# Performance work log

Hardware: AMD Instinct MI355X
Metric: run time of the kernel (lower is better)

Reference implementation:

```python
import jax, jax.numpy as jnp
import numpy as np

N_NODES = 200000
N_EDGES = 3200000
N_GRAPHS = 2000
N_MAX = 256   # max nodes per graph for dense batching (mean ~100)
K = 30        # SortAggregation k


def setup_inputs() -> dict:
    key = jax.random.key(0)
    ks = jax.random.split(key, 12)
    x = jax.random.normal(ks[0], (N_NODES, 128), jnp.float32)
    edge_index = jax.random.randint(ks[1], (2, N_EDGES), 0, N_NODES, dtype=jnp.int32)
    batch = jnp.sort(jax.random.randint(ks[2], (N_NODES,), 0, N_GRAPHS, dtype=jnp.int32))
    def lin(k, i, o):
        return (jax.random.normal(k, (i, o), jnp.float32) / np.sqrt(i)).astype(jnp.float32)
    return {
        'x': x, 'edge_index': edge_index, 'batch': batch,
        'W1': lin(ks[3], 128, 32), 'b1': jnp.zeros(32, jnp.float32),
        'W2': lin(ks[4], 32, 32),  'b2': jnp.zeros(32, jnp.float32),
        'W3': lin(ks[5], 32, 32),  'b3': jnp.zeros(32, jnp.float32),
        'W4': lin(ks[6], 32, 1),   'b4': jnp.zeros(1, jnp.float32),
        'cw5': (jax.random.normal(ks[7], (16, 1, 97), jnp.float32) / np.sqrt(97)).astype(jnp.float32),
        'cb5': jnp.zeros(16, jnp.float32),
        'cw6': (jax.random.normal(ks[8], (32, 16, 5), jnp.float32) / np.sqrt(80)).astype(jnp.float32),
        'cb6': jnp.zeros(32, jnp.float32),
        'fw1': lin(ks[9], 352, 128), 'fb1': jnp.zeros(128, jnp.float32),
        'fw2': lin(ks[10], 128, 10), 'fb2': jnp.zeros(10, jnp.float32),
    }


def _gcn_conv(h, W, b, src, dst, emask):
    # PyG GCNConv: remove self-loops handled via emask (weight 0), then add
    # self-loops weight 1; symmetric normalization D^{-1/2}(A+I)D^{-1/2} X W + b
    deg = jax.ops.segment_sum(emask, dst, num_segments=N_NODES) + 1.0  # + self loop
    dis = jax.lax.rsqrt(deg)  # deg >= 1 always, no inf
    norm = dis[src] * dis[dst] * emask  # [E]
    hw = h @ W                          # [N, out]
    agg = jax.ops.segment_sum(hw[src] * norm[:, None], dst, num_segments=N_NODES)
    agg = agg + hw * (dis * dis)[:, None]  # self-loop message
    return agg + b


def _sort_pool(x, batch):
    # PyG SortAggregation(k): dense-batch with fill = min-1, sort each graph by
    # last feature channel (descending), keep top-k rows, zero out padding, flatten.
    N, D = x.shape
    ones = jnp.ones((N,), jnp.int32)
    counts = jax.ops.segment_sum(ones, batch, num_segments=N_GRAPHS)
    offsets = jnp.concatenate([jnp.zeros((1,), jnp.int32), jnp.cumsum(counts)[:-1]])
    pos = jnp.arange(N, dtype=jnp.int32) - offsets[batch]  # batch is sorted
    fill = x.min() - 1.0
    dense = jnp.full((N_GRAPHS, N_MAX, D), fill, x.dtype).at[batch, pos].set(x)
    perm = jnp.argsort(-dense[:, :, -1], axis=1)            # descending by last channel
    dense = jnp.take_along_axis(dense, perm[:, :, None], axis=1)[:, :K]  # [G, K, D]
    dense = jnp.where(dense == fill, 0.0, dense)
    return dense.reshape(N_GRAPHS, K * D)


def _conv1d(x, w, b, stride):
    y = jax.lax.conv_general_dilated(x, w, window_strides=(stride,), padding='VALID',
                                     dimension_numbers=('NCH', 'OIH', 'NCH'))
    return y + b[None, :, None]


def reference(x, edge_index, batch, W1, b1, W2, b2, W3, b3, W4, b4,
              cw5, cb5, cw6, cb6, fw1, fb1, fw2, fb2):
    src, dst = edge_index[0], edge_index[1]
    emask = (src != dst).astype(x.dtype)  # remove_self_loops

    x1 = jnp.tanh(_gcn_conv(x,  W1, b1, src, dst, emask))
    x2 = jnp.tanh(_gcn_conv(x1, W2, b2, src, dst, emask))
    x3 = jnp.tanh(_gcn_conv(x2, W3, b3, src, dst, emask))
    x4 = jnp.tanh(_gcn_conv(x3, W4, b4, src, dst, emask))
    h = jnp.concatenate([x1, x2, x3, x4], axis=-1)  # [N, 97]

    p = _sort_pool(h, batch)                 # [G, 30*97]
    p = p[:, None, :]                        # [G, 1, 2910]
    p = jax.nn.relu(_conv1d(p, cw5, cb5, 97))  # [G, 16, 30]
    G = p.shape[0]
    p = p.reshape(G, 16, 15, 2).max(axis=-1)   # MaxPool1d(2,2) -> [G, 16, 15]
    p = jax.nn.relu(_conv1d(p, cw6, cb6, 1))   # [G, 32, 11]
    p = p.reshape(G, -1)                       # [G, 352]
    out = jax.nn.relu(p @ fw1 + fb1)           # dropout is identity at inference
    return jax.nn.log_softmax(out @ fw2 + fb2, axis=-1)
```

## Files before the change

### kernel.cpp

```cpp
#include <hip/hip_runtime.h>

#define N_NODESC 200000
#define N_EDGESC 3200000
#define N_GRAPHSC 2000
#define NMAXG 256
#define TOPK 30
#define DCAT 97
#define POOLW (TOPK*DCAT)
#define BUCKW 512
#define NBUCK ((N_NODESC+BUCKW-1)/BUCKW)
#define CAP 10240
#define PCHUNK 4096
#define NPBLK ((N_EDGESC+PCHUNK-1)/PCHUNK)

typedef int  iv4 __attribute__((ext_vector_type(4)));
typedef float fv4 __attribute__((ext_vector_type(4)));

__global__ __launch_bounds__(256) void k_part(const int* __restrict__ src, const int* __restrict__ dst,
                                              const int* __restrict__ batch, int* __restrict__ gcount,
                                              int* __restrict__ bcur, unsigned* __restrict__ pairbuf){
  __shared__ int hcnt[NBUCK];
  __shared__ int hbase[NBUCK];
  __shared__ int lofs[NBUCK];
  __shared__ int scan[256];
  __shared__ unsigned lbuf[PCHUNK];
  __shared__ unsigned short bbuf[PCHUNK];
  int blk = blockIdx.x, t = threadIdx.x;
  int nd = blk*256 + t;
  if (nd < N_NODESC) atomicAdd(&gcount[batch[nd]],1);
  int e0 = blk*PCHUNK;
  int e1 = e0 + PCHUNK; if (e1 > N_EDGESC) e1 = N_EDGESC;
  for (int i=t;i<NBUCK;i+=256) hcnt[i]=0;
  unsigned pk[16]; unsigned meta[16];
  __syncthreads();
  #pragma unroll
  for (int i=0;i<4;i++){
    int e = e0 + i*1024 + t*4;
    if (e < e1){
      iv4 d4 = __builtin_nontemporal_load((const iv4*)(dst+e));
      iv4 s4 = __builtin_nontemporal_load((const iv4*)(src+e));
      #pragma unroll
      for (int k=0;k<4;k++){
        int d = (k==0)?d4.x:(k==1)?d4.y:(k==2)?d4.z:d4.w;
        int s = (k==0)?s4.x:(k==1)?s4.y:(k==2)?s4.z:s4.w;
        if (s!=d){
          int bk = d>>9;
          int pl = atomicAdd(&hcnt[bk],1);
          pk[i*4+k]   = ((unsigned)(d&511)<<18)|(unsigned)s;
          meta[i*4+k] = ((unsigned)bk<<13)|(unsigned)pl;
        } else meta[i*4+k] = 0xFFFFFFFFu;
      }
    } else {
      #pragma unroll
      for (int k=0;k<4;k++) meta[i*4+k] = 0xFFFFFFFFu;
    }
  }
  __syncthreads();
  int i0=2*t, i1=2*t+1;
  int h0 = (i0<NBUCK)? hcnt[i0] : 0;
  int h1 = (i1<NBUCK)? hcnt[i1] : 0;
  int sp = h0+h1;
  scan[t]=sp; __syncthreads();
  for (int off=1;off<256;off<<=1){
    int u = (t>=off)? scan[t-off] : 0;
    __syncthreads();
    scan[t]+=u;
    __syncthreads();
  }
  int ex = scan[t]-sp;
  if (i0<NBUCK) lofs[i0]=ex;
  if (i1<NBUCK) lofs[i1]=ex+h0;
  for (int i=t;i<NBUCK;i+=256){
    int c = hcnt[i];
    hbase[i] = c ? (i*CAP + atomicAdd(&bcur[i],c)) : 0;
  }
  __syncthreads();
  #pragma unroll
  for (int k=0;k<16;k++){
    unsigned m = meta[k];
    if (m != 0xFFFFFFFFu){
      int bk = (int)(m>>13);
      int j = lofs[bk] + (int)(m & 0x1FFFu);
      lbuf[j] = pk[k];
      bbuf[j] = (unsigned short)bk;
    }
  }
  __syncthreads();
  int tot = lofs[NBUCK-1] + hcnt[NBUCK-1];
  for (int j=t; j<tot; j+=256){
    int bk = bbuf[j];
    int addr = hbase[bk] + (j - lofs[bk]);
    if (addr < (bk+1)*CAP) pairbuf[addr] = lbuf[j];
  }
}

__global__ __launch_bounds__(512) void k_bsort(const unsigned* __restrict__ pairbuf, const int* __restrict__ bcur,
                                               int* __restrict__ degc, int* __restrict__ offs,
                                               float* __restrict__ dis, int* __restrict__ csr){
  __shared__ int lcsr[CAP];
  __shared__ int lcnt[512];
  __shared__ int lofs[512];
  __shared__ int lcur[512];
  __shared__ int red[512];
  int b = blockIdx.x, t = threadIdx.x;
  int cnt_b = bcur[b]; if (cnt_b > CAP) cnt_b = CAP;
  int pv = 0;
  if (t < b){ int c = bcur[t]; if (c>CAP) c=CAP; pv = c; }
  red[t]=pv; __syncthreads();
  for (int off=256;off>0;off>>=1){ if (t<off) red[t]+=red[t+off]; __syncthreads(); }
  int base = red[0];
  const unsigned* pb = pairbuf + (size_t)b*CAP;
  lcnt[t]=0; __syncthreads();
  for (int i=t;i<cnt_b;i+=512) atomicAdd(&lcnt[pb[i]>>18],1);
  __syncthreads();
  lofs[t]=lcnt[t]; __syncthreads();
  for (int off=1;off<512;off<<=1){
    int u = (t>=off)? lofs[t-off] : 0;
    __syncthreads();
    lofs[t]+=u;
    __syncthreads();
  }
  int excl = lofs[t]-lcnt[t];
  int node = b*BUCKW + t;
  if (node < N_NODESC){
    degc[node] = lcnt[t];
    offs[node] = base + excl;
    dis[node]  = rsqrtf((float)lcnt[t] + 1.0f);
  }
  lcur[t]=excl;
  __syncthreads();
  for (int i=t;i<cnt_b;i+=512){
    unsigned v = pb[i];
    int p = atomicAdd(&lcur[v>>18],1);
    lcsr[p] = (int)(v & 0x3FFFFu);
  }
  __syncthreads();
  for (int i=t;i<cnt_b;i+=512) csr[base+i]=lcsr[i];
}

template<int KIN>
__global__ __launch_bounds__(256) void k_mm(const float* __restrict__ X, const float* __restrict__ W,
                                            const float* __restrict__ dis, float* __restrict__ out){
  __shared__ float xs[256*33];
  int r0 = blockIdx.x*256;
  int t = threadIdx.x;
  int r = r0 + t;
  float acc[32];
  #pragma unroll
  for (int f=0;f<32;f++) acc[f]=0.f;
  for (int kc=0; kc<KIN; kc+=32){
    __syncthreads();
    #pragma unroll
    for (int it=0; it<8; it++){
      int idx = it*256 + t;
      int row = idx>>3, c4 = idx&7;
      int gr = r0 + row;
      fv4 v = {0.f,0.f,0.f,0.f};
      if (gr < N_NODESC) v = __builtin_nontemporal_load((const fv4*)(X + (size_t)gr*KIN + kc + c4*4));
      int bofs = row*33 + c4*4;
      xs[bofs]=v.x; xs[bofs+1]=v.y; xs[bofs+2]=v.z; xs[bofs+3]=v.w;
    }
    __syncthreads();
    const float* w0 = W + kc*32;
    const float* xrow = xs + t*33;
    #pragma unroll
    for (int k=0;k<32;k++){
      float xv = xrow[k];
      #pragma unroll
      for (int f=0;f<32;f++) acc[f] = fmaf(xv, w0[k*32+f], acc[f]);
    }
  }
  if (r >= N_NODESC) return;
  float d = dis[r];
  float4* op = (float4*)(out + (size_t)r*32);
  #pragma unroll
  for (int f4=0;f4<8;f4++)
    op[f4] = make_float4(acc[4*f4]*d, acc[4*f4+1]*d, acc[4*f4+2]*d, acc[4*f4+3]*d);
}

__global__ __launch_bounds__(256) void k_agg(const float* __restrict__ hws, const int* __restrict__ csr,
                      const int* __restrict__ off, const int* __restrict__ cnt,
                      const float* __restrict__ dis, const float* __restrict__ bias,
                      float* __restrict__ out){
  int t = blockIdx.x*256 + threadIdx.x;
  int n = t>>5;
  if (n>=N_NODESC) return;
  int f = t&31;
  int beg = off[n], c = cnt[n];
  float a0=0.f,a1=0.f,a2=0.f,a3=0.f,a4=0.f,a5=0.f,a6=0.f,a7=0.f;
  for (int base=0; base<c; base+=32){
    int m = c-base; if (m>32) m=32;
    int idx = (f<m)? csr[beg+base+f] : 0;
    int j=0;
    for (; j+8<=m; j+=8){
      int s0=__shfl(idx,j,32),   s1=__shfl(idx,j+1,32),
          s2=__shfl(idx,j+2,32), s3=__shfl(idx,j+3,32),
          s4=__shfl(idx,j+4,32), s5=__shfl(idx,j+5,32),
          s6=__shfl(idx,j+6,32), s7=__shfl(idx,j+7,32);
      float v0=hws[(size_t)s0*32+f];
      float v1=hws[(size_t)s1*32+f];
      float v2=hws[(size_t)s2*32+f];
      float v3=hws[(size_t)s3*32+f];
      float v4=hws[(size_t)s4*32+f];
      float v5=hws[(size_t)s5*32+f];
      float v6=hws[(size_t)s6*32+f];
      float v7=hws[(size_t)s7*32+f];
      a0+=v0; a1+=v1; a2+=v2; a3+=v3; a4+=v4; a5+=v5; a6+=v6; a7+=v7;
    }
    for (; j+4<=m; j+=4){
      int s0=__shfl(idx,j,32), s1=__shfl(idx,j+1,32),
          s2=__shfl(idx,j+2,32), s3=__shfl(idx,j+3,32);
      float v0=hws[(size_t)s0*32+f];
      float v1=hws[(size_t)s1*32+f];
      float v2=hws[(size_t)s2*32+f];
      float v3=hws[(size_t)s3*32+f];
      a0+=v0; a1+=v1; a2+=v2; a3+=v3;
    }
    for (; j<m; j++){
      int s0=__shfl(idx,j,32);
      a0 += hws[(size_t)s0*32+f];
    }
  }
  float dn = dis[n];
  float sum = ((a0+a1)+(a2+a3)) + ((a4+a5)+(a6+a7));
  float v = dn*(sum+hws[(size_t)n*32+f]) + bias[f];
  out[(size_t)n*32+f] = tanhf(v);
}

__global__ __launch_bounds__(256) void k_aggF1(const float* __restrict__ hws, const int* __restrict__ csr,
                      const int* __restrict__ off, const int* __restrict__ cnt,
                      const float* __restrict__ dis, const float* __restrict__ bias,
                      const float* __restrict__ W4,
                      float* __restrict__ xout, float* __restrict__ hw4){
  __shared__ float Ws[32];
  int t = threadIdx.x;
  if (t<32) Ws[t]=W4[t];
  __syncthreads();
  int gt = blockIdx.x*256 + t;
  int n = gt>>5;
  if (n>=N_NODESC) return;
  int f = gt&31;
  int beg = off[n], c = cnt[n];
  float a0=0.f,a1=0.f,a2=0.f,a3=0.f,a4=0.f,a5=0.f,a6=0.f,a7=0.f;
  for (int base=0; base<c; base+=32){
    int m = c-base; if (m>32) m=32;
    int idx = (f<m)? csr[beg+base+f] : 0;
    int j=0;
    for (; j+8<=m; j+=8){
      int s0=__shfl(idx,j,32),   s1=__shfl(idx,j+1,32),
          s2=__shfl(idx,j+2,32), s3=__shfl(idx,j+3,32),
          s4=__shfl(idx,j+4,32), s5=__shfl(idx,j+5,32),
          s6=__shfl(idx,j+6,32), s7=__shfl(idx,j+7,32);
      float v0=hws[(size_t)s0*32+f];
      float v1=hws[(size_t)s1*32+f];
      float v2=hws[(size_t)s2*32+f];
      float v3=hws[(size_t)s3*32+f];
      float v4=hws[(size_t)s4*32+f];
      float v5=hws[(size_t)s5*32+f];
      float v6=hws[(size_t)s6*32+f];
      float v7=hws[(size_t)s7*32+f];
      a0+=v0; a1+=v1; a2+=v2; a3+=v3; a4+=v4; a5+=v5; a6+=v6; a7+=v7;
    }
    for (; j+4<=m; j+=4){
      int s0=__shfl(idx,j,32), s1=__shfl(idx,j+1,32),
          s2=__shfl(idx,j+2,32), s3=__shfl(idx,j+3,32);
      float v0=hws[(size_t)s0*32+f];
      float v1=hws[(size_t)s1*32+f];
      float v2=hws[(size_t)s2*32+f];
      float v3=hws[(size_t)s3*32+f];
      a0+=v0; a1+=v1; a2+=v2; a3+=v3;
    }
    for (; j<m; j++){
      int s0=__shfl(idx,j,32);
      a0 += hws[(size_t)s0*32+f];
    }
  }
  float dn = dis[n];
  float sum = ((a0+a1)+(a2+a3)) + ((a4+a5)+(a6+a7));
  float xv = tanhf(dn*(sum+hws[(size_t)n*32+f]) + bias[f]);
  xout[(size_t)n*32+f] = xv;
  float acc = xv*Ws[f];
  #pragma unroll
  for (int off2=16;off2>0;off2>>=1) acc += __shfl_xor(acc, off2, 32);
  if (f==0) hw4[n] = acc*dn;
}

__global__ void k_agg4(const float* __restrict__ hws4, const int* __restrict__ csr,
                       const int* __restrict__ off, const int* __restrict__ cnt,
                       const float* __restrict__ dis, const float* __restrict__ b4,
                       float* __restrict__ x4){
  int n = blockIdx.x*256+threadIdx.x;
  if (n>=N_NODESC) return;
  int beg=off[n], c=cnt[n];
  float a0=0.f,a1=0.f,a2=0.f,a3=0.f,a4=0.f,a5=0.f,a6=0.f,a7=0.f;
  int e=0;
  for (; e+8<=c; e+=8){
    int s0=csr[beg+e],   s1=csr[beg+e+1], s2=csr[beg+e+2], s3=csr[beg+e+3];
    int s4=csr[beg+e+4], s5=csr[beg+e+5], s6=csr[beg+e+6], s7=csr[beg+e+7];
    a0+=hws4[s0]; a1+=hws4[s1]; a2+=hws4[s2]; a3+=hws4[s3];
    a4+=hws4[s4]; a5+=hws4[s5]; a6+=hws4[s6]; a7+=hws4[s7];
  }
  for (; e<c; e++) a0+=hws4[csr[beg+e]];
  float dn=dis[n];
  float sum = ((a0+a1)+(a2+a3)) + ((a4+a5)+(a6+a7));
  x4[n] = tanhf(dn*(sum+hws4[n]) + b4[0]);
}

__global__ __launch_bounds__(256) void k_sortpool(const float* __restrict__ x1,const float* __restrict__ x2,const float* __restrict__ x3,const float* __restrict__ x4,
                           const int* __restrict__ gcount, float* __restrict__ pool){
  __shared__ float vals[NMAXG];
  __shared__ int sel[TOPK];
  __shared__ int redsum[256];
  int g = blockIdx.x;
  int t = threadIdx.x;
  int part = 0;
  for (int i=t; i<g; i+=256) part += gcount[i];
  redsum[t]=part; __syncthreads();
  for (int off=128;off>0;off>>=1){ if (t<off) redsum[t]+=redsum[t+off]; __syncthreads(); }
  int start = redsum[0];
  int cntg = gcount[g]; if (cntg>NMAXG) cntg=NMAXG;
  float v = 0.f;
  if (t<cntg) v = x4[start+t];
  vals[t] = v;
  __syncthreads();
  if (t<cntg){
    int rank=0;
    for (int j=0;j<cntg;j++){
      float vj=vals[j];
      rank += (vj>v) || (vj==v && j<t);
    }
    if (rank<TOPK) sel[rank]=t;
  }
  __syncthreads();
  int nsel = cntg<TOPK?cntg:TOPK;
  float* pg = pool + (size_t)g*POOLW;
  for (int idx=t; idx<POOLW; idx+=256){
    int r = idx/DCAT, c = idx - r*DCAT;
    float val=0.f;
    if (r<nsel){
      int node = start + sel[r];
      if (c<32) val = x1[(size_t)node*32+c];
      else if (c<64) val = x2[(size_t)node*32+(c-32)];
      else if (c<96) val = x3[(size_t)node*32+(c-64)];
      else val = x4[node];
    }
    pg[idx]=val;
  }
}

__global__ __launch_bounds__(128) void k_head(const float* __restrict__ pool,
                       const float* __restrict__ cw5, const float* __restrict__ cb5,
                       const float* __restrict__ cw6, const float* __restrict__ cb6,
                       const float* __restrict__ fw1, const float* __restrict__ fb1,
                       const float* __restrict__ fw2, const float* __restrict__ fb2,
                       float* __restrict__ out){
  __shared__ float P[POOLW];
  __shared__ float o5[16*30];
  __shared__ float m[16*15];
  __shared__ float o6[32*11];
  __shared__ float o1[128];
  __shared__ float logits[10];
  int g=blockIdx.x, t=threadIdx.x;
  const float* pg = pool + (size_t)g*POOLW;
  for (int i=t;i<POOLW;i+=128) P[i]=pg[i];
  __syncthreads();
  for (int i=t;i<480;i+=128){
    int o=i/30, k=i-o*30;
    float acc=cb5[o];
    const float* w=cw5+o*97;
    const float* p=P+k*97;
    for(int c=0;c<97;c++) acc = fmaf(p[c], w[c], acc);
    o5[o*30+k]=fmaxf(acc,0.f);
  }
  __syncthreads();
  for (int i=t;i<240;i+=128){
    int o=i/15,k=i-o*15;
    m[i]=fmaxf(o5[o*30+2*k], o5[o*30+2*k+1]);
  }
  __syncthreads();
  for (int i=t;i<352;i+=128){
    int o2=i/11, k=i-o2*11;
    float acc=cb6[o2];
    const float* w=cw6+o2*80;
    #pragma unroll
    for(int ii=0;ii<16;ii++)
      #pragma unroll
      for(int r=0;r<5;r++)
        acc = fmaf(m[ii*15+k+r], w[ii*5+r], acc);
    o6[o2*11+k]=fmaxf(acc,0.f);
  }
  __syncthreads();
  {
    float acc=fb1[t];
    for(int i=0;i<352;i++) acc = fmaf(o6[i], fw1[i*128+t], acc);
    o1[t]=fmaxf(acc,0.f);
  }
  __syncthreads();
  if (t<10){
    float acc=fb2[t];
    for(int j=0;j<128;j++) acc = fmaf(o1[j], fw2[j*10+t], acc);
    logits[t]=acc;
  }
  __syncthreads();
  if (t==0){
    float mx=logits[0];
    for(int c=1;c<10;c++) mx=fmaxf(mx,logits[c]);
    float s=0.f;
    for(int c=0;c<10;c++) s+=expf(logits[c]-mx);
    float lse=logf(s)+mx;
    for(int c=0;c<10;c++) out[(size_t)g*10+c]=logits[c]-lse;
  }
}

extern "C" void kernel_launch(void* const* d_in, const int* in_sizes, int n_in,
                              void* d_out, int out_size, void* d_ws, size_t ws_size,
                              hipStream_t stream){
  const float* x    = (const float*)d_in[0];
  const int*   ei   = (const int*)d_in[1];
  const int*   batch= (const int*)d_in[2];
  const float* W1=(const float*)d_in[3]; const float* b1=(const float*)d_in[4];
  const float* W2=(const float*)d_in[5]; const float* b2=(const float*)d_in[6];
  const float* W3=(const float*)d_in[7]; const float* b3=(const float*)d_in[8];
  const float* W4=(const float*)d_in[9]; const float* b4=(const float*)d_in[10];
  const float* cw5=(const float*)d_in[11]; const float* cb5=(const float*)d_in[12];
  const float* cw6=(const float*)d_in[13]; const float* cb6=(const float*)d_in[14];
  const float* fw1=(const float*)d_in[15]; const float* fb1=(const float*)d_in[16];
  const float* fw2=(const float*)d_in[17]; const float* fb2=(const float*)d_in[18];
  float* out=(float*)d_out;
  const int* src = ei;
  const int* dst = ei + N_EDGESC;

  char* ws=(char*)d_ws;
  size_t o=0;
  auto alloc=[&](size_t nbytes)->char*{ char* p=ws+o; o += (nbytes+255)&~(size_t)255; return p; };
  float* dis    = (float*)alloc((size_t)N_NODESC*4);
  int*   offs   = (int*)alloc((size_t)N_NODESC*4);
  int*   degc   = (int*)alloc((size_t)N_NODESC*4);
  int*   bcur   = (int*)alloc((size_t)NBUCK*4);
  int*   gcount = (int*)alloc((size_t)N_GRAPHSC*4);
  unsigned* pairbuf = (unsigned*)alloc((size_t)NBUCK*CAP*4);
  int*   csr    = (int*)alloc((size_t)N_EDGESC*4);
  float* x1 = (float*)alloc((size_t)N_NODESC*32*4);
  float* x2 = (float*)alloc((size_t)N_NODESC*32*4);
  float* x3 = (float*)alloc((size_t)N_NODESC*32*4);
  float* x4 = (float*)alloc((size_t)N_NODESC*4);
  float* hw = (float*)alloc((size_t)N_NODESC*32*4);
  float* hw4 = (float*)alloc((size_t)N_NODESC*4);
  float* pool = hw;

  size_t mset = (((size_t)NBUCK*4+255)&~(size_t)255) + (size_t)N_GRAPHSC*4;
  (void)hipMemsetAsync(bcur, 0, mset, stream);

  int gN = (N_NODESC+255)/256;

  k_part<<<NPBLK,256,0,stream>>>(src,dst,batch,gcount,bcur,pairbuf);
  k_bsort<<<NBUCK,512,0,stream>>>(pairbuf,bcur,degc,offs,dis,csr);

  int gMM=(N_NODESC+7)/8;
  k_mm<128><<<gN,256,0,stream>>>(x, W1, dis, hw);
  k_agg<<<gMM,256,0,stream>>>(hw,csr,offs,degc,dis,b1,x1);
  k_mm<32><<<gN,256,0,stream>>>(x1, W2, dis, hw);
  k_agg<<<gMM,256,0,stream>>>(hw,csr,offs,degc,dis,b2,x2);
  k_mm<32><<<gN,256,0,stream>>>(x2, W3, dis, hw);
  k_aggF1<<<gMM,256,0,stream>>>(hw,csr,offs,degc,dis,b3,W4,x3,hw4);
  k_agg4<<<gN,256,0,stream>>>(hw4,csr,offs,degc,dis,b4,x4);

  k_sortpool<<<N_GRAPHSC,256,0,stream>>>(x1,x2,x3,x4,gcount,pool);
  k_head<<<N_GRAPHSC,128,0,stream>>>(pool,cw5,cb5,cw6,cb6,fw1,fb1,fw2,fb2,out);
}
```

Measured before the change: 477.8 us.

## Fuse layer-4 aggregation, sort pooling and head into one per-graph kernel

Layer-4 aggregation, sort pooling and the conv/MLP head now run in one kernel with one block per graph. The pooled tensor stays in shared memory instead of going through a global buffer, and the x4 array is dropped. This removes two kernel launches and the global write and re-read of the pool matrix. In exchange, per-node layer-4 aggregation is serialized inside graph blocks and shared memory per block grows, which may reduce occupancy.

Result: no change. 477.0 us (-0.2%).

```diff
diff --git a/kernel.cpp b/kernel.cpp
--- a/kernel.cpp
+++ b/kernel.cpp
@@ -285,44 +285,46 @@
   if (f==0) hw4[n] = acc*dn;
 }
 
-__global__ void k_agg4(const float* __restrict__ hws4, const int* __restrict__ csr,
-                       const int* __restrict__ off, const int* __restrict__ cnt,
+__global__ __launch_bounds__(256) void k_tail(const float* __restrict__ x1,const float* __restrict__ x2,const float* __restrict__ x3,
+                       const float* __restrict__ hw4, const int* __restrict__ csr,
+                       const int* __restrict__ offs, const int* __restrict__ degc,
                        const float* __restrict__ dis, const float* __restrict__ b4,
-                       float* __restrict__ x4){
-  int n = blockIdx.x*256+threadIdx.x;
-  if (n>=N_NODESC) return;
-  int beg=off[n], c=cnt[n];
-  float a0=0.f,a1=0.f,a2=0.f,a3=0.f,a4=0.f,a5=0.f,a6=0.f,a7=0.f;
-  int e=0;
-  for (; e+8<=c; e+=8){
-    int s0=csr[beg+e],   s1=csr[beg+e+1], s2=csr[beg+e+2], s3=csr[beg+e+3];
-    int s4=csr[beg+e+4], s5=csr[beg+e+5], s6=csr[beg+e+6], s7=csr[beg+e+7];
-    a0+=hws4[s0]; a1+=hws4[s1]; a2+=hws4[s2]; a3+=hws4[s3];
-    a4+=hws4[s4]; a5+=hws4[s5]; a6+=hws4[s6]; a7+=hws4[s7];
-  }
-  for (; e<c; e++) a0+=hws4[csr[beg+e]];
-  float dn=dis[n];
-  float sum = ((a0+a1)+(a2+a3)) + ((a4+a5)+(a6+a7));
-  x4[n] = tanhf(dn*(sum+hws4[n]) + b4[0]);
-}
-
-__global__ __launch_bounds__(256) void k_sortpool(const float* __restrict__ x1,const float* __restrict__ x2,const float* __restrict__ x3,const float* __restrict__ x4,
-                           const int* __restrict__ gcount, float* __restrict__ pool){
+                       const int* __restrict__ gcount,
+                       const float* __restrict__ cw5, const float* __restrict__ cb5,
+                       const float* __restrict__ cw6, const float* __restrict__ cb6,
+                       const float* __restrict__ fw1, const float* __restrict__ fb1,
+                       const float* __restrict__ fw2, const float* __restrict__ fb2,
+                       float* __restrict__ out){
   __shared__ float vals[NMAXG];
   __shared__ int sel[TOPK];
   __shared__ int redsum[256];
-  int g = blockIdx.x;
-  int t = threadIdx.x;
-  int part = 0;
-  for (int i=t; i<g; i+=256) part += gcount[i];
+  __shared__ float P[POOLW];
+  __shared__ float o5[16*30];
+  __shared__ float m[16*15];
+  __shared__ float o6[32*11];
+  __shared__ float o1[128];
+  __shared__ float logits[10];
+  int g=blockIdx.x, t=threadIdx.x;
+  int part=0;
+  for (int i=t;i<g;i+=256) part += gcount[i];
   redsum[t]=part; __syncthreads();
   for (int off=128;off>0;off>>=1){ if (t<off) redsum[t]+=redsum[t+off]; __syncthreads(); }
   int start = redsum[0];
   int cntg = gcount[g]; if (cntg>NMAXG) cntg=NMAXG;
-  float v = 0.f;
-  if (t<cntg) v = x4[start+t];
-  vals[t] = v;
-  __syncthreads();
+  float v=0.f;
+  if (t<cntg){
+    int n = start+t;
+    int beg=offs[n], c=degc[n];
+    float a0=0.f,a1=0.f,a2=0.f,a3=0.f;
+    int e=0;
+    for (; e+4<=c; e+=4){
+      int s0=csr[beg+e], s1=csr[beg+e+1], s2=csr[beg+e+2], s3=csr[beg+e+3];
+      a0+=hw4[s0]; a1+=hw4[s1]; a2+=hw4[s2]; a3+=hw4[s3];
+    }
+    for (; e<c; e++) a0+=hw4[csr[beg+e]];
+    v = tanhf(dis[n]*(((a0+a1)+(a2+a3))+hw4[n]) + b4[0]);
+  }
+  vals[t]=v; __syncthreads();
   if (t<cntg){
     int rank=0;
     for (int j=0;j<cntg;j++){
@@ -333,7 +335,6 @@
   }
   __syncthreads();
   int nsel = cntg<TOPK?cntg:TOPK;
-  float* pg = pool + (size_t)g*POOLW;
   for (int idx=t; idx<POOLW; idx+=256){
     int r = idx/DCAT, c = idx - r*DCAT;
     float val=0.f;
@@ -342,29 +343,12 @@
       if (c<32) val = x1[(size_t)node*32+c];
       else if (c<64) val = x2[(size_t)node*32+(c-32)];
       else if (c<96) val = x3[(size_t)node*32+(c-64)];
-      else val = x4[node];
-    }
-    pg[idx]=val;
-  }
-}
-
-__global__ __launch_bounds__(128) void k_head(const float* __restrict__ pool,
-                       const float* __restrict__ cw5, const float* __restrict__ cb5,
-                       const float* __restrict__ cw6, const float* __restrict__ cb6,
-                       const float* __restrict__ fw1, const float* __restrict__ fb1,
-                       const float* __restrict__ fw2, const float* __restrict__ fb2,
-                       float* __restrict__ out){
-  __shared__ float P[POOLW];
-  __shared__ float o5[16*30];
-  __shared__ float m[16*15];
-  __shared__ float o6[32*11];
-  __shared__ float o1[128];
-  __shared__ float logits[10];
-  int g=blockIdx.x, t=threadIdx.x;
-  const float* pg = pool + (size_t)g*POOLW;
-  for (int i=t;i<POOLW;i+=128) P[i]=pg[i];
-  __syncthreads();
-  for (int i=t;i<480;i+=128){
+      else val = vals[sel[r]];
+    }
+    P[idx]=val;
+  }
+  __syncthreads();
+  for (int i=t;i<480;i+=256){
     int o=i/30, k=i-o*30;
     float acc=cb5[o];
     const float* w=cw5+o*97;
@@ -373,12 +357,12 @@
     o5[o*30+k]=fmaxf(acc,0.f);
   }
   __syncthreads();
-  for (int i=t;i<240;i+=128){
+  for (int i=t;i<240;i+=256){
     int o=i/15,k=i-o*15;
     m[i]=fmaxf(o5[o*30+2*k], o5[o*30+2*k+1]);
   }
   __syncthreads();
-  for (int i=t;i<352;i+=128){
+  for (int i=t;i<352;i+=256){
     int o2=i/11, k=i-o2*11;
     float acc=cb6[o2];
     const float* w=cw6+o2*80;
@@ -390,7 +374,7 @@
     o6[o2*11+k]=fmaxf(acc,0.f);
   }
   __syncthreads();
-  {
+  if (t<128){
     float acc=fb1[t];
     for(int i=0;i<352;i++) acc = fmaf(o6[i], fw1[i*128+t], acc);
     o1[t]=fmaxf(acc,0.f);
@@ -443,10 +427,8 @@
   float* x1 = (float*)alloc((size_t)N_NODESC*32*4);
   float* x2 = (float*)alloc((size_t)N_NODESC*32*4);
   float* x3 = (float*)alloc((size_t)N_NODESC*32*4);
-  float* x4 = (float*)alloc((size_t)N_NODESC*4);
   float* hw = (float*)alloc((size_t)N_NODESC*32*4);
   float* hw4 = (float*)alloc((size_t)N_NODESC*4);
-  float* pool = hw;
 
   size_t mset = (((size_t)NBUCK*4+255)&~(size_t)255) + (size_t)N_GRAPHSC*4;
   (void)hipMemsetAsync(bcur, 0, mset, stream);
@@ -463,8 +445,7 @@
   k_agg<<<gMM,256,0,stream>>>(hw,csr,offs,degc,dis,b2,x2);
   k_mm<32><<<gN,256,0,stream>>>(x2, W3, dis, hw);
   k_aggF1<<<gMM,256,0,stream>>>(hw,csr,offs,degc,dis,b3,W4,x3,hw4);
-  k_agg4<<<gN,256,0,stream>>>(hw4,csr,offs,degc,dis,b4,x4);
-
-  k_sortpool<<<N_GRAPHSC,256,0,stream>>>(x1,x2,x3,x4,gcount,pool);
-  k_head<<<N_GRAPHSC,128,0,stream>>>(pool,cw5,cb5,cw6,cb6,fw1,fb1,fw2,fb2,out);
-}
+
+  k_tail<<<N_GRAPHSC,256,0,stream>>>(x1,x2,x3,hw4,csr,offs,degc,dis,b4,gcount,
+                                     cw5,cb5,cw6,cb6,fw1,fb1,fw2,fb2,out);
+}
```
